# Kernel optimization log

Hardware: AMD Instinct MI355X
Metric: run time of the kernel (lower is better)

## Reference

```python
import jax, jax.numpy as jnp
import numpy as np
from jax import lax

B, L, D, DM, S, M, P = 8, 2048, 512, 1024, 32, 4, 4096


def setup_inputs() -> dict:
    key = jax.random.key(0)
    ks = jax.random.split(key, 13)
    emb = jax.random.normal(ks[0], (B, L, D), jnp.float32)
    pos = jax.random.randint(ks[1], (B, L), 1, P + 1)          # pos >= 1 (0 reserved for CLS)
    sid = jax.random.randint(ks[2], (B, L), 0, S)
    mod = jax.random.randint(ks[3], (B, L), 0, M)
    role = jax.random.randint(ks[4], (B, L), 0, 3)
    padding_mask = jax.random.uniform(ks[5], (B, L)) < 0.9
    W_proj = jax.random.normal(ks[6], (S, DM, D), jnp.float32) / np.float32(np.sqrt(D))
    b_proj = jax.random.normal(ks[7], (S, DM), jnp.float32) * 0.01
    cls_content = jax.random.normal(ks[8], (DM,), jnp.float32)
    pos_emb = jax.random.normal(ks[9], (P + 1, DM), jnp.float32) * 0.02
    id_emb = jax.random.normal(ks[10], (S + 1, DM), jnp.float32) * 0.02
    mod_emb = jax.random.normal(ks[11], (M, DM), jnp.float32) * 0.02
    role_emb = jax.random.normal(ks[12], (3, DM), jnp.float32) * 0.02
    return dict(emb=emb, pos=pos, sid=sid, mod=mod, role=role, padding_mask=padding_mask,
                W_proj=W_proj, b_proj=b_proj, cls_content=cls_content,
                pos_emb=pos_emb, id_emb=id_emb, mod_emb=mod_emb, role_emb=role_emb)


def _moe_project(emb, sid, padding_mask, W_proj, b_proj):
    """Per-token per-signal Linear: tokens[b,l] = W_proj[sid[b,l]] @ emb[b,l] + b_proj[sid[b,l]].
    Computed as S dense GEMMs masked per token (dense-dispatch MoE), avoiding an
    O(B*L*DM*D) gathered-weight tensor."""
    def step(acc, sWb):
        s, W, b = sWb
        y = jnp.einsum('bld,od->blo', emb, W) + b  # (B, L, DM)
        m = (sid == s) & padding_mask              # padded tokens stay zero
        return acc + jnp.where(m[..., None], y, 0.0), None
    acc0 = jnp.zeros(emb.shape[:2] + (W_proj.shape[1],), emb.dtype)
    acc, _ = lax.scan(step, acc0, (jnp.arange(W_proj.shape[0]), W_proj, b_proj))
    return acc


def reference(emb, pos, sid, mod, role, padding_mask,
              W_proj, b_proj, cls_content, pos_emb, id_emb, mod_emb, role_emb):
    Bc, Lc = pos.shape
    dm = cls_content.shape[0]
    cls_id = id_emb.shape[0] - 1  # == num_signals

    proj = _moe_project(emb, sid, padding_mask, W_proj, b_proj)  # (B, L, DM)

    cls = jnp.broadcast_to(cls_content, (Bc, 1, dm))
    tokens = jnp.concatenate([cls, proj], axis=1)                # (B, L+1, DM)

    pos_full = jnp.concatenate([jnp.zeros((Bc, 1), pos.dtype), pos], axis=1)
    sid_full = jnp.concatenate([jnp.full((Bc, 1), cls_id, sid.dtype), sid], axis=1)
    tokens = tokens + pos_emb[pos_full] + id_emb[sid_full]

    # modality + role embeddings only on non-CLS tokens (added even where padded, as in torch)
    tokens = tokens.at[:, 1:, :].add(mod_emb[mod] + role_emb[role])

    attn_keep = jnp.concatenate([jnp.ones((Bc, 1), bool), padding_mask], axis=1)
    return tokens, attn_keep
```

## Files before the change

### kernel.cpp

```cpp
#include <hip/hip_runtime.h>
#include <hip/hip_bf16.h>


#define NB   8
#define NL   2048
#define ND   512
#define NDM  1024
#define NS   32
#define NTOK (NB * NL)
#define LP1  (NL + 1)
#define MAXTILES 160
#define EXP_CAP 1024
#define EMB_ELEMS (NTOK * ND)
#define W_ELEMS (NS * NDM * ND)

static __device__ __forceinline__ size_t attn_off() { return (size_t)NB * LP1 * NDM; }

typedef __attribute__((ext_vector_type(8))) short bf16x8;
typedef __attribute__((ext_vector_type(4))) float f32x4;

__device__ __forceinline__ unsigned short f2bf(float f) {
    unsigned int x = __float_as_uint(f);
    x += 0x7fffu + ((x >> 16) & 1u);
    return (unsigned short)(x >> 16);
}

__device__ __forceinline__ bf16x8 cvt8(float4 a, float4 b) {
    bf16x8 r;
    r[0] = (short)f2bf(a.x); r[1] = (short)f2bf(a.y);
    r[2] = (short)f2bf(a.z); r[3] = (short)f2bf(a.w);
    r[4] = (short)f2bf(b.x); r[5] = (short)f2bf(b.y);
    r[6] = (short)f2bf(b.z); r[7] = (short)f2bf(b.w);
    return r;
}

__device__ __forceinline__ float4 ld4(const float* p) { return *(const float4*)p; }
__device__ __forceinline__ float4 add4(float4 a, float4 b) {
    return make_float4(a.x + b.x, a.y + b.y, a.z + b.z, a.w + b.w);
}

__device__ __forceinline__ void gl_lds16(const void* g, void* l) {
    __builtin_amdgcn_global_load_lds((const __attribute__((address_space(1))) void*)g,
                                     (__attribute__((address_space(3))) void*)l, 16, 0, 0);
}

__global__ void k_bucket(const int* __restrict__ sid, const int* __restrict__ mask,
                         const int* __restrict__ pos, const int* __restrict__ mod,
                         const int* __restrict__ role,
                         int* __restrict__ cnt, int* __restrict__ restCnt,
                         int* __restrict__ tokList, int* __restrict__ restList,
                         float* __restrict__ out) {
    int t = blockIdx.x * 256 + threadIdx.x;
    if (t >= NTOK) return;
    int s = sid[t];
    bool keep = mask[t] != 0;
    int b = t >> 11, l = t & (NL - 1);
    out[attn_off() + (size_t)b * LP1 + l + 1] = keep ? 1.0f : 0.0f;
    if (t < NB) out[attn_off() + (size_t)t * LP1] = 1.0f;
    int mr = mod[t] * 3 + role[t];
    int packed = t | (pos[t] << 14) | (mr << 27);
    if (keep) {
        int idx = atomicAdd(&cnt[s], 1);
        if (idx < EXP_CAP) tokList[s * EXP_CAP + idx] = packed;
    } else {
        int ridx = atomicAdd(restCnt, 1);
        restList[ridx] = packed;
    }
}

__global__ void k_tiles(const int* __restrict__ cnt, int* __restrict__ meta,
                        int4* __restrict__ tiles,
                        const float* __restrict__ me, const float* __restrict__ re,
                        float* __restrict__ mrT) {
    if (threadIdx.x == 0) {
        int idx = 0;
        for (int e = 0; e < NS; ++e) {
            int c = min(cnt[e], EXP_CAP);
            for (int r = 0; r < c; r += 128)
                tiles[idx++] = make_int4(e, r, min(128, c - r), 0);
        }
        meta[0] = idx;
    }
    for (int i = threadIdx.x; i < 12 * (NDM / 4); i += 256) {
        int mr = i / (NDM / 4); int o = (i % (NDM / 4)) * 4;
        int m = mr / 3, ro = mr % 3;
        float4 v = add4(ld4(me + (size_t)m * NDM + o), ld4(re + (size_t)ro * NDM + o));
        *(float4*)&mrT[(size_t)mr * NDM + o] = v;
    }
}

__global__ void k_cvt(const float* __restrict__ emb, const float* __restrict__ W,
                      short* __restrict__ embBf, short* __restrict__ wBf) {
    size_t i = ((size_t)blockIdx.x * 256 + threadIdx.x) * 16;
    const float* src; short* dst;
    if (i < (size_t)EMB_ELEMS) { src = emb + i; dst = embBf + i; }
    else { src = W + (i - EMB_ELEMS); dst = wBf + (i - EMB_ELEMS); }
    float4 a = ld4(src), b = ld4(src + 4), c = ld4(src + 8), d = ld4(src + 12);
    *(bf16x8*)dst       = cvt8(a, b);
    *(bf16x8*)(dst + 8) = cvt8(c, d);
}

__global__ __launch_bounds__(256) void k_gemm(
    const short* __restrict__ embBf, const short* __restrict__ wBf,
    const int* __restrict__ tokList, const int4* __restrict__ tiles,
    const int* __restrict__ meta,
    const float* __restrict__ bp, const float* __restrict__ pe,
    const float* __restrict__ ie, const float* __restrict__ mrT,
    float* __restrict__ out) {
    if (blockIdx.x >= meta[0]) return;
    int4 td = tiles[blockIdx.x];
    const int e = td.x, rowBase = td.y, nRows = td.z;
    const int nBase = blockIdx.y * 128;

    __shared__ short As[2][128 * 32];
    __shared__ short Bs[2][128 * 32];

    const int tid  = threadIdx.x;
    const int lane = tid & 63;
    const int w    = tid >> 6;
    const int wr   = w >> 1, wc = w & 1;
    const int fr   = lane & 15, kg = lane >> 4;

    const int srow = lane >> 2;
    const int schunk = lane & 3;
    const short* aBase[2]; const short* bBase[2]; int qa[2];
#pragma unroll
    for (int c = 0; c < 2; ++c) {
        int q = w * 2 + c; qa[c] = q;
        int row = q * 16 + srow;
        int ar = (row < nRows) ? row : 0;
        int pk = tokList[(size_t)e * EXP_CAP + rowBase + ar];
        int tok = pk & 16383;
        aBase[c] = embBf + (size_t)tok * ND + schunk * 8;
        bBase[c] = wBf + ((size_t)e * NDM + nBase + row) * ND + schunk * 8;
    }

    const float* bpE = bp + (size_t)e * NDM;
    const float* ieE = ie + (size_t)e * NDM;
    float eb[4]; int colv[4];
#pragma unroll
    for (int j = 0; j < 4; ++j) {
        colv[j] = nBase + wc * 64 + j * 16 + fr;
        eb[j] = bpE[colv[j]] + ieE[colv[j]];
    }

    f32x4 acc[4][4];
#pragma unroll
    for (int i = 0; i < 4; ++i)
#pragma unroll
        for (int j = 0; j < 4; ++j)
            acc[i][j] = (f32x4){0.f, 0.f, 0.f, 0.f};

#define STAGE(buf, ks) do {                                            \
        _Pragma("unroll")                                              \
        for (int c = 0; c < 2; ++c)                                    \
            gl_lds16(aBase[c] + (ks) * 32, &As[buf][qa[c] * 512]);     \
        _Pragma("unroll")                                              \
        for (int c = 0; c < 2; ++c)                                    \
            gl_lds16(bBase[c] + (ks) * 32, &Bs[buf][qa[c] * 512]);     \
    } while (0)

    STAGE(0, 0);
    for (int ks = 0; ks < ND / 32; ++ks) {
        const int cur = ks & 1;
        if (ks < ND / 32 - 1) {
            STAGE(cur ^ 1, ks + 1);
            asm volatile("s_waitcnt vmcnt(4)" ::: "memory");
        } else {
            asm volatile("s_waitcnt vmcnt(0)" ::: "memory");
        }
        __builtin_amdgcn_s_barrier();
        asm volatile("" ::: "memory");
        bf16x8 af[4], bv[4];
#pragma unroll
        for (int i = 0; i < 4; ++i)
            af[i] = *(const bf16x8*)&As[cur][(wr * 64 + i * 16 + fr) * 32 + kg * 8];
#pragma unroll
        for (int j = 0; j < 4; ++j)
            bv[j] = *(const bf16x8*)&Bs[cur][(wc * 64 + j * 16 + fr) * 32 + kg * 8];
#pragma unroll
        for (int i = 0; i < 4; ++i)
#pragma unroll
            for (int j = 0; j < 4; ++j)
                acc[i][j] = __builtin_amdgcn_mfma_f32_16x16x32_bf16(af[i], bv[j], acc[i][j], 0, 0, 0);
        asm volatile("" ::: "memory");
        __builtin_amdgcn_s_barrier();
        asm volatile("" ::: "memory");
    }
#undef STAGE

#pragma unroll
    for (int i = 0; i < 4; ++i) {
#pragma unroll
        for (int r = 0; r < 4; ++r) {
            int row = wr * 64 + i * 16 + kg * 4 + r;
            if (row < nRows) {
                int pk = tokList[(size_t)e * EXP_CAP + rowBase + row];
                int t = pk & 16383, p = (pk >> 14) & 8191, mr = (pk >> 27) & 15;
                const float* peR = pe + (size_t)p * NDM;
                const float* mrR = mrT + (size_t)mr * NDM;
                size_t orow = ((size_t)(t >> 11) * LP1 + (t & (NL - 1)) + 1) * NDM;
#pragma unroll
                for (int j = 0; j < 4; ++j)
                    out[orow + colv[j]] = acc[i][j][r] + eb[j] + peR[colv[j]] + mrR[colv[j]];
            }
        }
    }
}

__global__ void k_rest(const int* __restrict__ sid,
                       const int* __restrict__ restList, const int* __restrict__ meta,
                       const float* __restrict__ cls_c, const float* __restrict__ pos_e,
                       const float* __restrict__ id_e, const float* __restrict__ mrT,
                       float* __restrict__ out) {
    int total = meta[1] + NB;
    int half = threadIdx.x >> 7;
    int o = (threadIdx.x & 127) * 8;
    for (int rI = blockIdx.x * 2 + half; rI < total; rI += gridDim.x * 2) {
        float4 v0, v1; size_t orow;
        if (rI < NB) {
            const float* ieC = id_e + (size_t)NS * NDM;
            v0 = add4(add4(ld4(cls_c + o), ld4(pos_e + o)), ld4(ieC + o));
            v1 = add4(add4(ld4(cls_c + o + 4), ld4(pos_e + o + 4)), ld4(ieC + o + 4));
            orow = (size_t)rI * LP1 * NDM;
        } else {
            int pk = restList[rI - NB];
            int t = pk & 16383, p = (pk >> 14) & 8191, mr = (pk >> 27) & 15;
            int s = sid[t];
            const float* peR = pos_e + (size_t)p * NDM;
            const float* ieR = id_e + (size_t)s * NDM;
            const float* mrR = mrT + (size_t)mr * NDM;
            v0 = add4(add4(ld4(peR + o), ld4(ieR + o)), ld4(mrR + o));
            v1 = add4(add4(ld4(peR + o + 4), ld4(ieR + o + 4)), ld4(mrR + o + 4));
            orow = ((size_t)(t >> 11) * LP1 + (t & (NL - 1)) + 1) * NDM;
        }
        *(float4*)&out[orow + o] = v0;
        *(float4*)&out[orow + o + 4] = v1;
    }
}

extern "C" void kernel_launch(void* const* d_in, const int* in_sizes, int n_in,
                              void* d_out, int out_size, void* d_ws, size_t ws_size,
                              hipStream_t stream) {
    const float* emb  = (const float*)d_in[0];
    const int* pos    = (const int*)d_in[1];
    const int* sid    = (const int*)d_in[2];
    const int* mod    = (const int*)d_in[3];
    const int* role   = (const int*)d_in[4];
    const int* mask   = (const int*)d_in[5];
    const float* Wp   = (const float*)d_in[6];
    const float* bp   = (const float*)d_in[7];
    const float* cls  = (const float*)d_in[8];
    const float* pe   = (const float*)d_in[9];
    const float* ie   = (const float*)d_in[10];
    const float* me   = (const float*)d_in[11];
    const float* re   = (const float*)d_in[12];
    float* out = (float*)d_out;

    int* ws        = (int*)d_ws;
    int* cnt       = ws;
    int* meta      = ws + 32;
    int4* tiles    = (int4*)(ws + 128);
    int* tokList   = ws + 1024;
    int* restList  = ws + 33792;
    float* mrT     = (float*)(ws + 50176);
    short* embBf   = (short*)((char*)d_ws + 262144);
    short* wBf     = (short*)((char*)d_ws + 262144 + (size_t)EMB_ELEMS * 2);

    hipMemsetAsync(ws, 0, 64 * sizeof(int), stream);
    k_bucket<<<NTOK / 256, 256, 0, stream>>>(sid, mask, pos, mod, role,
                                             cnt, meta + 1, tokList, restList, out);
    k_tiles<<<1, 256, 0, stream>>>(cnt, meta, tiles, me, re, mrT);
    k_cvt<<<(EMB_ELEMS + W_ELEMS) / (256 * 16), 256, 0, stream>>>(emb, Wp, embBf, wBf);

    dim3 gg(MAXTILES, NDM / 128);
    k_gemm<<<gg, 256, 0, stream>>>(embBf, wBf, tokList, tiles, meta,
                                   bp, pe, ie, mrT, out);
    k_rest<<<512, 256, 0, stream>>>(sid, restList, meta, cls, pe, ie, mrT, out);
}
```

Baseline: 134.0 us.

## Enlarge expert GEMM tile to 256x256 with BK=64 and XOR-swizzled LDS

The grouped expert GEMM now uses 256-row by 256-column tiles with a K step of 64. It runs 512 threads (8 waves, each computing a 128x64 sub-tile) and holds 128 KB of double-buffered LDS, with dynamic shared memory raised via a function attribute. LDS chunks are XOR-swizzled by row to avoid bank conflicts on the wider rows. The aim is more operand reuse and fewer redundant global and LDS loads per MFMA. The cost is fewer blocks, about one per CU, with only one block resident because of the LDS size, which reduces latency hiding and parallelism.

```diff
diff --git a/kernel.cpp b/kernel.cpp
--- a/kernel.cpp
+++ b/kernel.cpp
@@ -9,7 +9,7 @@
 #define NS   32
 #define NTOK (NB * NL)
 #define LP1  (NL + 1)
-#define MAXTILES 160
+#define MAXTILES 96
 #define EXP_CAP 1024
 #define EMB_ELEMS (NTOK * ND)
 #define W_ELEMS (NS * NDM * ND)
@@ -76,8 +76,8 @@
         int idx = 0;
         for (int e = 0; e < NS; ++e) {
             int c = min(cnt[e], EXP_CAP);
-            for (int r = 0; r < c; r += 128)
-                tiles[idx++] = make_int4(e, r, min(128, c - r), 0);
+            for (int r = 0; r < c; r += 256)
+                tiles[idx++] = make_int4(e, r, min(256, c - r), 0);
         }
         meta[0] = idx;
     }
@@ -100,7 +100,7 @@
     *(bf16x8*)(dst + 8) = cvt8(c, d);
 }
 
-__global__ __launch_bounds__(256) void k_gemm(
+__global__ __launch_bounds__(512, 2) void k_gemm(
     const short* __restrict__ embBf, const short* __restrict__ wBf,
     const int* __restrict__ tokList, const int4* __restrict__ tiles,
     const int* __restrict__ meta,
@@ -108,31 +108,29 @@
     const float* __restrict__ ie, const float* __restrict__ mrT,
     float* __restrict__ out) {
     if (blockIdx.x >= meta[0]) return;
+    extern __shared__ short lds[];
     int4 td = tiles[blockIdx.x];
     const int e = td.x, rowBase = td.y, nRows = td.z;
-    const int nBase = blockIdx.y * 128;
-
-    __shared__ short As[2][128 * 32];
-    __shared__ short Bs[2][128 * 32];
+    const int nBase = blockIdx.y * 256;
 
     const int tid  = threadIdx.x;
     const int lane = tid & 63;
     const int w    = tid >> 6;
-    const int wr   = w >> 1, wc = w & 1;
+    const int wr   = w >> 2, wc = w & 3;
     const int fr   = lane & 15, kg = lane >> 4;
-
-    const int srow = lane >> 2;
-    const int schunk = lane & 3;
-    const short* aBase[2]; const short* bBase[2]; int qa[2];
-#pragma unroll
-    for (int c = 0; c < 2; ++c) {
-        int q = w * 2 + c; qa[c] = q;
-        int row = q * 16 + srow;
-        int ar = (row < nRows) ? row : 0;
-        int pk = tokList[(size_t)e * EXP_CAP + rowBase + ar];
-        int tok = pk & 16383;
-        aBase[c] = embBf + (size_t)tok * ND + schunk * 8;
-        bBase[c] = wBf + ((size_t)e * NDM + nBase + row) * ND + schunk * 8;
+    const int xs   = fr & 7;
+    const int c0   = kg ^ xs;
+
+    const int srow = lane >> 3;
+    const int schunk = (lane & 7) ^ srow;
+    const short* aSrc[4]; const short* bSrc[4];
+#pragma unroll
+    for (int q = 0; q < 4; ++q) {
+        int r = (w * 4 + q) * 8 + srow;
+        int ar = (r < nRows) ? r : 0;
+        int tok = tokList[(size_t)e * EXP_CAP + rowBase + ar] & 16383;
+        aSrc[q] = embBf + (size_t)tok * ND + schunk * 8;
+        bSrc[q] = wBf + ((size_t)e * NDM + nBase + r) * ND + schunk * 8;
     }
 
     const float* bpE = bp + (size_t)e * NDM;
@@ -144,56 +142,64 @@
         eb[j] = bpE[colv[j]] + ieE[colv[j]];
     }
 
-    f32x4 acc[4][4];
-#pragma unroll
-    for (int i = 0; i < 4; ++i)
+    f32x4 acc[8][4];
+#pragma unroll
+    for (int i = 0; i < 8; ++i)
 #pragma unroll
         for (int j = 0; j < 4; ++j)
             acc[i][j] = (f32x4){0.f, 0.f, 0.f, 0.f};
 
-#define STAGE(buf, ks) do {                                            \
-        _Pragma("unroll")                                              \
-        for (int c = 0; c < 2; ++c)                                    \
-            gl_lds16(aBase[c] + (ks) * 32, &As[buf][qa[c] * 512]);     \
-        _Pragma("unroll")                                              \
-        for (int c = 0; c < 2; ++c)                                    \
-            gl_lds16(bBase[c] + (ks) * 32, &Bs[buf][qa[c] * 512]);     \
+#define STAGE(buf, kt) do {                                              \
+        const int bo_ = (buf) * 16384;                                   \
+        _Pragma("unroll")                                                \
+        for (int q = 0; q < 4; ++q) {                                    \
+            gl_lds16(aSrc[q] + (kt) * 64, lds + bo_ + (w * 4 + q) * 512);\
+            gl_lds16(bSrc[q] + (kt) * 64, lds + 32768 + bo_ + (w * 4 + q) * 512);\
+        }                                                                \
     } while (0)
 
     STAGE(0, 0);
-    for (int ks = 0; ks < ND / 32; ++ks) {
-        const int cur = ks & 1;
-        if (ks < ND / 32 - 1) {
-            STAGE(cur ^ 1, ks + 1);
-            asm volatile("s_waitcnt vmcnt(4)" ::: "memory");
+    for (int kt = 0; kt < ND / 64; ++kt) {
+        const int buf = kt & 1;
+        if (kt < ND / 64 - 1) {
+            STAGE(buf ^ 1, kt + 1);
+            asm volatile("s_waitcnt vmcnt(8)" ::: "memory");
         } else {
             asm volatile("s_waitcnt vmcnt(0)" ::: "memory");
         }
         __builtin_amdgcn_s_barrier();
         asm volatile("" ::: "memory");
-        bf16x8 af[4], bv[4];
-#pragma unroll
-        for (int i = 0; i < 4; ++i)
-            af[i] = *(const bf16x8*)&As[cur][(wr * 64 + i * 16 + fr) * 32 + kg * 8];
-#pragma unroll
-        for (int j = 0; j < 4; ++j)
-            bv[j] = *(const bf16x8*)&Bs[cur][(wc * 64 + j * 16 + fr) * 32 + kg * 8];
-#pragma unroll
-        for (int i = 0; i < 4; ++i)
+        const short* Aq = lds + buf * 16384;
+        const short* Bq = lds + 32768 + buf * 16384;
+        bf16x8 bfr[4][2];
+#pragma unroll
+        for (int j = 0; j < 4; ++j) {
+            int base = (wc * 64 + j * 16 + fr) * 64;
+            bfr[j][0] = *(const bf16x8*)&Bq[base + c0 * 8];
+            bfr[j][1] = *(const bf16x8*)&Bq[base + (c0 ^ 4) * 8];
+        }
+#pragma unroll
+        for (int i = 0; i < 8; ++i) {
+            int base = (wr * 128 + i * 16 + fr) * 64;
+            bf16x8 a0 = *(const bf16x8*)&Aq[base + c0 * 8];
+            bf16x8 a1 = *(const bf16x8*)&Aq[base + (c0 ^ 4) * 8];
 #pragma unroll
             for (int j = 0; j < 4; ++j)
-                acc[i][j] = __builtin_amdgcn_mfma_f32_16x16x32_bf16(af[i], bv[j], acc[i][j], 0, 0, 0);
+                acc[i][j] = __builtin_amdgcn_mfma_f32_16x16x32_bf16(a0, bfr[j][0], acc[i][j], 0, 0, 0);
+#pragma unroll
+            for (int j = 0; j < 4; ++j)
+                acc[i][j] = __builtin_amdgcn_mfma_f32_16x16x32_bf16(a1, bfr[j][1], acc[i][j], 0, 0, 0);
+        }
         asm volatile("" ::: "memory");
         __builtin_amdgcn_s_barrier();
-        asm volatile("" ::: "memory");
     }
 #undef STAGE
 
 #pragma unroll
-    for (int i = 0; i < 4; ++i) {
+    for (int i = 0; i < 8; ++i) {
 #pragma unroll
         for (int r = 0; r < 4; ++r) {
-            int row = wr * 64 + i * 16 + kg * 4 + r;
+            int row = wr * 128 + i * 16 + kg * 4 + r;
             if (row < nRows) {
                 int pk = tokList[(size_t)e * EXP_CAP + rowBase + row];
                 int t = pk & 16383, p = (pk >> 14) & 8191, mr = (pk >> 27) & 15;
@@ -267,14 +273,21 @@
     short* embBf   = (short*)((char*)d_ws + 262144);
     short* wBf     = (short*)((char*)d_ws + 262144 + (size_t)EMB_ELEMS * 2);
 
+    static int lds_attr_set = 0;
+    if (!lds_attr_set) {
+        hipFuncSetAttribute((const void*)k_gemm,
+                            hipFuncAttributeMaxDynamicSharedMemorySize, 131072);
+        lds_attr_set = 1;
+    }
+
     hipMemsetAsync(ws, 0, 64 * sizeof(int), stream);
     k_bucket<<<NTOK / 256, 256, 0, stream>>>(sid, mask, pos, mod, role,
                                              cnt, meta + 1, tokList, restList, out);
     k_tiles<<<1, 256, 0, stream>>>(cnt, meta, tiles, me, re, mrT);
     k_cvt<<<(EMB_ELEMS + W_ELEMS) / (256 * 16), 256, 0, stream>>>(emb, Wp, embBf, wBf);
 
-    dim3 gg(MAXTILES, NDM / 128);
-    k_gemm<<<gg, 256, 0, stream>>>(embBf, wBf, tokList, tiles, meta,
-                                   bp, pe, ie, mrT, out);
+    dim3 gg(MAXTILES, NDM / 256);
+    k_gemm<<<gg, 512, 131072, stream>>>(embBf, wBf, tokList, tiles, meta,
+                                        bp, pe, ie, mrT, out);
     k_rest<<<512, 256, 0, stream>>>(sid, restList, meta, cls, pe, ie, mrT, out);
 }
```

After: 147.2 us. 1.1x slower.

## Replace direct global-to-LDS loads with register-staged single-buffer LDS and XOR swizzle

Applied to the files above, without the earlier changes.

The GEMM kernel stops using global_load_lds double buffering and instead prefetches the next K-slice into registers while computing on a single LDS buffer. LDS writes and reads use an XOR swizzle on the 16-byte chunk index to avoid bank conflicts. Launch bounds now request 3 blocks per CU, helped by the halved LDS footprint. The cost is two barriers per K step and more register pressure from the prefetched fragments.

```diff
diff --git a/kernel.cpp b/kernel.cpp
--- a/kernel.cpp
+++ b/kernel.cpp
@@ -37,11 +37,6 @@
 __device__ __forceinline__ float4 ld4(const float* p) { return *(const float4*)p; }
 __device__ __forceinline__ float4 add4(float4 a, float4 b) {
     return make_float4(a.x + b.x, a.y + b.y, a.z + b.z, a.w + b.w);
-}
-
-__device__ __forceinline__ void gl_lds16(const void* g, void* l) {
-    __builtin_amdgcn_global_load_lds((const __attribute__((address_space(1))) void*)g,
-                                     (__attribute__((address_space(3))) void*)l, 16, 0, 0);
 }
 
 __global__ void k_bucket(const int* __restrict__ sid, const int* __restrict__ mask,
@@ -100,7 +95,7 @@
     *(bf16x8*)(dst + 8) = cvt8(c, d);
 }
 
-__global__ __launch_bounds__(256) void k_gemm(
+__global__ __launch_bounds__(256, 3) void k_gemm(
     const short* __restrict__ embBf, const short* __restrict__ wBf,
     const int* __restrict__ tokList, const int4* __restrict__ tiles,
     const int* __restrict__ meta,
@@ -112,8 +107,8 @@
     const int e = td.x, rowBase = td.y, nRows = td.z;
     const int nBase = blockIdx.y * 128;
 
-    __shared__ short As[2][128 * 32];
-    __shared__ short Bs[2][128 * 32];
+    __shared__ short SA[128 * 32];
+    __shared__ short SB[128 * 32];
 
     const int tid  = threadIdx.x;
     const int lane = tid & 63;
@@ -121,19 +116,19 @@
     const int wr   = w >> 1, wc = w & 1;
     const int fr   = lane & 15, kg = lane >> 4;
 
-    const int srow = lane >> 2;
-    const int schunk = lane & 3;
-    const short* aBase[2]; const short* bBase[2]; int qa[2];
-#pragma unroll
-    for (int c = 0; c < 2; ++c) {
-        int q = w * 2 + c; qa[c] = q;
-        int row = q * 16 + srow;
-        int ar = (row < nRows) ? row : 0;
-        int pk = tokList[(size_t)e * EXP_CAP + rowBase + ar];
-        int tok = pk & 16383;
-        aBase[c] = embBf + (size_t)tok * ND + schunk * 8;
-        bBase[c] = wBf + ((size_t)e * NDM + nBase + row) * ND + schunk * 8;
-    }
+    const int srow = tid >> 2;
+    const int sch  = tid & 3;
+    const size_t eBase = (size_t)e * EXP_CAP + rowBase;
+    int ar0 = (srow < nRows) ? srow : 0;
+    int ar1 = (srow + 64 < nRows) ? srow + 64 : 0;
+    int tok0 = tokList[eBase + ar0] & 16383;
+    int tok1 = tokList[eBase + ar1] & 16383;
+    const short* a0 = embBf + (size_t)tok0 * ND + sch * 8;
+    const short* a1 = embBf + (size_t)tok1 * ND + sch * 8;
+    const short* b0 = wBf + ((size_t)e * NDM + nBase + srow) * ND + sch * 8;
+    const short* b1 = wBf + ((size_t)e * NDM + nBase + srow + 64) * ND + sch * 8;
+    const int wo0 = srow * 32 + (sch ^ ((srow >> 1) & 3)) * 8;
+    const int wo1 = wo0 + 64 * 32;
 
     const float* bpE = bp + (size_t)e * NDM;
     const float* ieE = ie + (size_t)e * NDM;
@@ -151,43 +146,38 @@
         for (int j = 0; j < 4; ++j)
             acc[i][j] = (f32x4){0.f, 0.f, 0.f, 0.f};
 
-#define STAGE(buf, ks) do {                                            \
-        _Pragma("unroll")                                              \
-        for (int c = 0; c < 2; ++c)                                    \
-            gl_lds16(aBase[c] + (ks) * 32, &As[buf][qa[c] * 512]);     \
-        _Pragma("unroll")                                              \
-        for (int c = 0; c < 2; ++c)                                    \
-            gl_lds16(bBase[c] + (ks) * 32, &Bs[buf][qa[c] * 512]);     \
-    } while (0)
-
-    STAGE(0, 0);
+    bf16x8 ra0 = *(const bf16x8*)a0;
+    bf16x8 ra1 = *(const bf16x8*)a1;
+    bf16x8 rb0 = *(const bf16x8*)b0;
+    bf16x8 rb1 = *(const bf16x8*)b1;
+
+    const int pc = kg ^ ((fr >> 1) & 3);
     for (int ks = 0; ks < ND / 32; ++ks) {
-        const int cur = ks & 1;
+        __syncthreads();
+        *(bf16x8*)&SA[wo0] = ra0;
+        *(bf16x8*)&SA[wo1] = ra1;
+        *(bf16x8*)&SB[wo0] = rb0;
+        *(bf16x8*)&SB[wo1] = rb1;
+        __syncthreads();
         if (ks < ND / 32 - 1) {
-            STAGE(cur ^ 1, ks + 1);
-            asm volatile("s_waitcnt vmcnt(4)" ::: "memory");
-        } else {
-            asm volatile("s_waitcnt vmcnt(0)" ::: "memory");
-        }
-        __builtin_amdgcn_s_barrier();
-        asm volatile("" ::: "memory");
+            ra0 = *(const bf16x8*)(a0 + (ks + 1) * 32);
+            ra1 = *(const bf16x8*)(a1 + (ks + 1) * 32);
+            rb0 = *(const bf16x8*)(b0 + (ks + 1) * 32);
+            rb1 = *(const bf16x8*)(b1 + (ks + 1) * 32);
+        }
         bf16x8 af[4], bv[4];
 #pragma unroll
         for (int i = 0; i < 4; ++i)
-            af[i] = *(const bf16x8*)&As[cur][(wr * 64 + i * 16 + fr) * 32 + kg * 8];
+            af[i] = *(const bf16x8*)&SA[(wr * 64 + i * 16 + fr) * 32 + pc * 8];
 #pragma unroll
         for (int j = 0; j < 4; ++j)
-            bv[j] = *(const bf16x8*)&Bs[cur][(wc * 64 + j * 16 + fr) * 32 + kg * 8];
+            bv[j] = *(const bf16x8*)&SB[(wc * 64 + j * 16 + fr) * 32 + pc * 8];
 #pragma unroll
         for (int i = 0; i < 4; ++i)
 #pragma unroll
             for (int j = 0; j < 4; ++j)
                 acc[i][j] = __builtin_amdgcn_mfma_f32_16x16x32_bf16(af[i], bv[j], acc[i][j], 0, 0, 0);
-        asm volatile("" ::: "memory");
-        __builtin_amdgcn_s_barrier();
-        asm volatile("" ::: "memory");
-    }
-#undef STAGE
+    }
 
 #pragma unroll
     for (int i = 0; i < 4; ++i) {
@@ -195,7 +185,7 @@
         for (int r = 0; r < 4; ++r) {
             int row = wr * 64 + i * 16 + kg * 4 + r;
             if (row < nRows) {
-                int pk = tokList[(size_t)e * EXP_CAP + rowBase + row];
+                int pk = tokList[eBase + row];
                 int t = pk & 16383, p = (pk >> 14) & 8191, mr = (pk >> 27) & 15;
                 const float* peR = pe + (size_t)p * NDM;
                 const float* mrR = mrT + (size_t)mr * NDM;
```

Result: no change. 134.5 us (+0.4%).
